# Performance work log

Hardware: AMD Instinct MI355X
Metric: run time of the kernel (lower is better)

## Reference

```python
import jax, jax.numpy as jnp
import numpy as np

BOUND = 1.0
MIN_NEAR = 0.05
NUM_STEPS = 64
UP_STEPS = 64
DENSITY_SCALE = 1.0
N_RAYS = 16384
HIDDEN = 64


def setup_inputs() -> dict:
    key = jax.random.key(0)
    ks = jax.random.split(key, 8)
    # cameras hover near z=2 looking roughly toward -z so rays hit the [-1,1]^3 AABB
    rays_o = jax.random.normal(ks[0], (N_RAYS, 3), jnp.float32) * 0.1 + jnp.array([0.0, 0.0, 2.0])
    rays_d = jax.random.normal(ks[1], (N_RAYS, 3), jnp.float32) * 0.2 + jnp.array([0.0, 0.0, -1.0])
    rays_d = rays_d / jnp.linalg.norm(rays_d, axis=-1, keepdims=True)
    W1 = jax.random.normal(ks[2], (3, HIDDEN), jnp.float32) / jnp.sqrt(3.0)
    b1 = jnp.zeros((HIDDEN,), jnp.float32)
    w_sigma = jax.random.normal(ks[3], (HIDDEN, 1), jnp.float32) / jnp.sqrt(float(HIDDEN))
    b_sigma = jnp.zeros((1,), jnp.float32)
    W_rgb = jax.random.normal(ks[4], (HIDDEN, 3), jnp.float32) / jnp.sqrt(float(HIDDEN))
    b_rgb = jnp.zeros((3,), jnp.float32)
    return {"rays_o": rays_o, "rays_d": rays_d, "W1": W1, "b1": b1,
            "w_sigma": w_sigma, "b_sigma": b_sigma, "W_rgb": W_rgb, "b_rgb": b_rgb}


def near_far_cube(rays_o, rays_d, bound, min_near):
    tmin = (-bound - rays_o) / (rays_d + 1e-15)
    tmax = (bound - rays_o) / (rays_d + 1e-15)
    near = jnp.max(jnp.minimum(tmin, tmax), axis=-1, keepdims=True)
    far = jnp.min(jnp.maximum(tmin, tmax), axis=-1, keepdims=True)
    miss = far < near
    near = jnp.where(miss, 1e9, near)
    far = jnp.where(miss, 1e9, far)
    near = jnp.maximum(near, min_near)
    return near, far


def sample_pdf(bins, weights, n_samples):
    # bins: [N, M+1], weights: [N, M]; deterministic (det=True) inverse-CDF sampling
    weights = weights + 1e-5
    pdf = weights / jnp.sum(weights, -1, keepdims=True)
    cdf = jnp.cumsum(pdf, -1)
    cdf = jnp.concatenate([jnp.zeros_like(cdf[..., :1]), cdf], -1)  # [N, M+1]
    u = jnp.linspace(0.5 / n_samples, 1.0 - 0.5 / n_samples, n_samples, dtype=cdf.dtype)
    u = jnp.broadcast_to(u, cdf.shape[:-1] + (n_samples,))
    inds = jax.vmap(lambda c, uu: jnp.searchsorted(c, uu, side='right'))(cdf, u)
    below = jnp.maximum(inds - 1, 0)
    above = jnp.minimum(inds, cdf.shape[-1] - 1)
    cdf_b = jnp.take_along_axis(cdf, below, -1)
    cdf_a = jnp.take_along_axis(cdf, above, -1)
    bins_b = jnp.take_along_axis(bins, below, -1)
    bins_a = jnp.take_along_axis(bins, above, -1)
    denom = cdf_a - cdf_b
    denom = jnp.where(denom < 1e-5, jnp.ones_like(denom), denom)
    t = (u - cdf_b) / denom
    return bins_b + t * (bins_a - bins_b)


def mlp(pts, W1, b1, w_sigma, b_sigma, W_rgb, b_rgb):
    h = jax.nn.relu(pts @ W1 + b1)                      # [N, T, HIDDEN]
    sigma = jax.nn.softplus(h @ w_sigma + b_sigma)[..., 0]  # [N, T]
    rgb = jax.nn.sigmoid(h @ W_rgb + b_rgb)             # [N, T, 3]
    return sigma, rgb


def alpha_composite_weights(z_vals, sigma, sample_dist):
    deltas = z_vals[..., 1:] - z_vals[..., :-1]
    deltas = jnp.concatenate([deltas, jnp.broadcast_to(sample_dist, deltas[..., :1].shape)], -1)
    alphas = 1.0 - jnp.exp(-deltas * DENSITY_SCALE * sigma)
    trans = jnp.cumprod(jnp.concatenate([jnp.ones_like(alphas[..., :1]), 1.0 - alphas + 1e-15], -1)[..., :-1], -1)
    return alphas * trans


def reference(rays_o, rays_d, W1, b1, w_sigma, b_sigma, W_rgb, b_rgb):
    rays_d = rays_d / jnp.linalg.norm(rays_d, axis=-1, keepdims=True)
    near, far = near_far_cube(rays_o, rays_d, BOUND, MIN_NEAR)  # [N,1]
    sample_dist = (far - near) / NUM_STEPS                      # [N,1]

    # coarse stratified (deterministic) samples
    z = jnp.linspace(0.0, 1.0, NUM_STEPS, dtype=rays_o.dtype)
    z_vals = near + (far - near) * z                            # [N,T]
    xyzs = rays_o[:, None, :] + rays_d[:, None, :] * z_vals[..., None]
    xyzs = jnp.clip(xyzs, -BOUND, BOUND)
    sigma, _ = mlp(xyzs, W1, b1, w_sigma, b_sigma, W_rgb, b_rgb)
    weights = alpha_composite_weights(z_vals, sigma, sample_dist)

    # inverse-CDF importance resampling (no-grad in original)
    z_mid = 0.5 * (z_vals[..., :-1] + z_vals[..., 1:])          # [N,T-1]
    new_z = sample_pdf(z_mid, weights[:, 1:-1], UP_STEPS)       # [N,UP]
    new_z = jax.lax.stop_gradient(new_z)

    z_all = jnp.sort(jnp.concatenate([z_vals, new_z], -1), -1)  # [N,T+UP]
    xyzs_all = rays_o[:, None, :] + rays_d[:, None, :] * z_all[..., None]
    xyzs_all = jnp.clip(xyzs_all, -BOUND, BOUND)
    sigma_all, rgb_all = mlp(xyzs_all, W1, b1, w_sigma, b_sigma, W_rgb, b_rgb)
    weights_all = alpha_composite_weights(z_all, sigma_all, sample_dist)

    weights_sum = jnp.sum(weights_all, -1)                      # [N]
    image = jnp.sum(weights_all[..., None] * rgb_all, axis=-2)  # [N,3]
    image = image + (1.0 - weights_sum)[..., None]              # white background
    return image
```

## Files before the change

kernel.cpp:

```cpp
#include <hip/hip_runtime.h>
#include <math.h>

#define WAVES_PER_BLOCK 4

typedef float v2f __attribute__((ext_vector_type(2)));
typedef float v4f __attribute__((ext_vector_type(4)));
typedef __fp16 fp16v2 __attribute__((ext_vector_type(2)));
typedef _Float16 half8 __attribute__((ext_vector_type(8)));

__device__ __forceinline__ v2f v2_fma(v2f a, v2f b, v2f c) {
    return __builtin_elementwise_fma(a, b, c);
}
__device__ __forceinline__ v2f v2_max0(v2f a) {
    return __builtin_elementwise_max(a, (v2f){0.0f, 0.0f});
}
__device__ __forceinline__ v2f v2_splat(float x) { return (v2f){x, x}; }

__device__ __forceinline__ float fast_rcp(float x) { return __builtin_amdgcn_rcpf(x); }

#define DPP_ROW_SHR(n)  (0x110 | (n))
#define DPP_WF_SL1      0x130
#define DPP_WF_SR1      0x138
#define DPP_ROW_BCAST15 0x142
#define DPP_ROW_BCAST31 0x143

template <int CTRL, int RM = 0xf, int BM = 0xf, bool BC = false>
__device__ __forceinline__ float fdpp(float old_, float src) {
    return __int_as_float(__builtin_amdgcn_update_dpp(
        __float_as_int(old_), __float_as_int(src), CTRL, RM, BM, BC));
}

__device__ __forceinline__ float lane63_bcast(float x) {
    return __int_as_float(__builtin_amdgcn_readlane(__float_as_int(x), 63));
}

__device__ __forceinline__ float scan_add_dpp(float x) {
    x += fdpp<DPP_ROW_SHR(1)>(0.0f, x);
    x += fdpp<DPP_ROW_SHR(2)>(0.0f, x);
    x += fdpp<DPP_ROW_SHR(4)>(0.0f, x);
    x += fdpp<DPP_ROW_SHR(8)>(0.0f, x);
    x += fdpp<DPP_ROW_BCAST15, 0xa>(0.0f, x);
    x += fdpp<DPP_ROW_BCAST31, 0xc>(0.0f, x);
    return x;
}
__device__ __forceinline__ float scan_mul_dpp(float x) {
    x *= fdpp<DPP_ROW_SHR(1)>(1.0f, x);
    x *= fdpp<DPP_ROW_SHR(2)>(1.0f, x);
    x *= fdpp<DPP_ROW_SHR(4)>(1.0f, x);
    x *= fdpp<DPP_ROW_SHR(8)>(1.0f, x);
    x *= fdpp<DPP_ROW_BCAST15, 0xa>(1.0f, x);
    x *= fdpp<DPP_ROW_BCAST31, 0xc>(1.0f, x);
    return x;
}
__device__ __forceinline__ float wave_sum_dpp(float x) {
    return lane63_bcast(scan_add_dpp(x));
}

__device__ __forceinline__ float softplus_f(float x) {
    return fmaxf(x, 0.0f) + __logf(1.0f + __expf(-fabsf(x)));
}
__device__ __forceinline__ float sigmoid_f(float x) {
    return fast_rcp(1.0f + __expf(-x));
}
__device__ __forceinline__ float clamp1(float x) {
    return fminf(fmaxf(x, -1.0f), 1.0f);
}

__device__ __forceinline__ int count_lt64(const float* a, float x) {
    int lo = 0, hi = 64;
    while (lo < hi) { int mid = (lo + hi) >> 1; if (a[mid] < x) lo = mid + 1; else hi = mid; }
    return lo;
}
__device__ __forceinline__ int count_le64(const float* a, float x) {
    int lo = 0, hi = 64;
    while (lo < hi) { int mid = (lo + hi) >> 1; if (a[mid] <= x) lo = mid + 1; else hi = mid; }
    return lo;
}

__device__ __forceinline__ half8 build_afrag(const v2f* cr, const v2f* mr, v2f zz, int q) {
    union { half8 h; fp16v2 p[4]; } af;
#pragma unroll
    for (int g4 = 0; g4 < 4; ++g4) {
        v2f hp = v2_max0(v2_fma(mr[q * 4 + g4], zz, cr[q * 4 + g4]));
        af.p[g4] = __builtin_amdgcn_cvt_pkrtz(hp.x, hp.y);
    }
    return af.h;
}

__global__ __launch_bounds__(WAVES_PER_BLOCK * 64, 4)
void nerf_render_kernel(const float* __restrict__ rays_o,
                        const float* __restrict__ rays_d,
                        const float* __restrict__ W1,
                        const float* __restrict__ b1,
                        const float* __restrict__ w_sigma,
                        const float* __restrict__ b_sigma,
                        const float* __restrict__ W_rgb,
                        const float* __restrict__ b_rgb,
                        float* __restrict__ out)
{
    const int tid  = threadIdx.x;
    const int lane = tid & 63;
    const int wv   = tid >> 6;
    const int ray  = blockIdx.x * WAVES_PER_BLOCK + wv;
    const int r15  = lane & 15;
    const int kgrp = lane >> 4;

    __shared__ float s_cm  [WAVES_PER_BLOCK][128];
    __shared__ float s_sig [WAVES_PER_BLOCK][64];
    __shared__ float s_zmid[WAVES_PER_BLOCK][64];
    __shared__ float s_cdf [WAVES_PER_BLOCK][64];
    __shared__ float s_zall[WAVES_PER_BLOCK][128];
    __shared__ float s_out [WAVES_PER_BLOCK][4 * 132];

    half8 bfrag[2];
#pragma unroll
    for (int q = 0; q < 2; ++q) {
#pragma unroll
        for (int j = 0; j < 8; ++j) {
            int k = q * 32 + kgrp * 8 + j;
            float wval = 0.0f;
            if (r15 == 0)      wval = w_sigma[k];
            else if (r15 < 4)  wval = W_rgb[3 * k + (r15 - 1)];
            bfrag[q][j] = (_Float16)wval;
        }
    }

    float ox = rays_o[ray * 3 + 0], oy = rays_o[ray * 3 + 1], oz = rays_o[ray * 3 + 2];
    float dx = rays_d[ray * 3 + 0], dy = rays_d[ray * 3 + 1], dz = rays_d[ray * 3 + 2];
    {
        float inv = __builtin_amdgcn_rsqf(dx * dx + dy * dy + dz * dz);
        dx *= inv; dy *= inv; dz *= inv;
    }

    float rx = fast_rcp(dx + 1e-15f);
    float ry = fast_rcp(dy + 1e-15f);
    float rz = fast_rcp(dz + 1e-15f);
    float t0x = (-1.0f - ox) * rx, t1x = (1.0f - ox) * rx;
    float t0y = (-1.0f - oy) * ry, t1y = (1.0f - oy) * ry;
    float t0z = (-1.0f - oz) * rz, t1z = (1.0f - oz) * rz;
    float nearv = fmaxf(fmaxf(fminf(t0x, t1x), fminf(t0y, t1y)), fminf(t0z, t1z));
    float farv  = fminf(fminf(fmaxf(t0x, t1x), fmaxf(t0y, t1y)), fmaxf(t0z, t1z));
    const bool miss = (farv < nearv);
    if (miss) { nearv = 1e9f; farv = 1e9f; }
    nearv = fmaxf(nearv, 0.05f);
    const float sample_dist = (farv - nearv) * (1.0f / 64.0f);

    const float bs0 = b_sigma[0];
    const float br0 = b_rgb[0], br1 = b_rgb[1], br2 = b_rgb[2];

    {
        float w1x = W1[lane], w1y = W1[64 + lane], w1z = W1[128 + lane];
        float eox = ox, eoy = oy, eoz = oz, msc = 1.0f;
        if (miss) {
            eox = clamp1(fmaf(dx, 1e9f, ox));
            eoy = clamp1(fmaf(dy, 1e9f, oy));
            eoz = clamp1(fmaf(dz, 1e9f, oz));
            msc = 0.0f;
        }
        float cj = fmaf(eox, w1x, fmaf(eoy, w1y, fmaf(eoz, w1z, b1[lane])));
        float mj = msc * fmaf(dx, w1x, fmaf(dy, w1y, dz * w1z));
        int g = (lane >> 1) * 4 + (lane & 1);
        s_cm[wv][g]     = cj;
        s_cm[wv][g + 2] = mj;
    }

    v2f cr[8], mr[8];
#pragma unroll
    for (int q = 0; q < 2; ++q) {
#pragma unroll
        for (int g4 = 0; g4 < 4; ++g4) {
            v4f g = *(const v4f*)&s_cm[wv][4 * (q * 16 + kgrp * 4 + g4)];
            cr[q * 4 + g4] = (v2f){g.x, g.y};
            mr[q * 4 + g4] = (v2f){g.z, g.w};
        }
    }

    const float biasv = (r15 == 0) ? bs0 : (r15 == 1) ? br0 : (r15 == 2) ? br1
                       : (r15 == 3) ? br2 : 0.0f;
    const v4f accInit = (v4f){biasv, biasv, biasv, biasv};

    const float stepz = (farv - nearv) * (1.0f / 63.0f);
#pragma unroll
    for (int mt = 0; mt < 4; ++mt) {
        float zs = fminf(fmaf(stepz, (float)(mt * 16 + r15), nearv), 6.0e4f);
        v2f zz = v2_splat(zs);
        v4f acc = accInit;
        acc = __builtin_amdgcn_mfma_f32_16x16x32_f16(build_afrag(cr, mr, zz, 0), bfrag[0], acc, 0, 0, 0);
        acc = __builtin_amdgcn_mfma_f32_16x16x32_f16(build_afrag(cr, mr, zz, 1), bfrag[1], acc, 0, 0, 0);
        if (r15 == 0) {
            *(v4f*)&s_sig[wv][mt * 16 + kgrp * 4] = acc;
        }
    }
    float sigma = softplus_f(s_sig[wv][lane]);

    float z = nearv + (farv - nearv) * ((float)lane * (1.0f / 63.0f));

    float z_next = fdpp<DPP_WF_SL1>(0.0f, z);
    float delta  = (lane < 63) ? (z_next - z) : sample_dist;
    float alpha  = 1.0f - __expf(-delta * sigma);
    float v      = 1.0f - alpha + 1e-15f;
    float incl   = scan_mul_dpp(v);
    float trans  = fdpp<DPP_WF_SR1>(1.0f, incl);
    float w = alpha * trans;

    float wgt = (lane >= 1 && lane <= 62) ? (w + 1e-5f) : 0.0f;
    float cumw = scan_add_dpp(wgt);
    float total = lane63_bcast(cumw);
    float cdf_incl = cumw * fast_rcp(total);

    float zmid = 0.5f * (z + z_next);
    s_zmid[wv][lane] = (lane < 63) ? zmid : 0.0f;
    s_cdf [wv][lane] = (lane < 63) ? cdf_incl : 2.0f;

    float u = 0.0078125f + (float)lane * 0.015625f;
    int ind = count_le64(s_cdf[wv], u);
    int below = ind - 1;
    int above = (ind < 62) ? ind : 62;
    float cb = s_cdf[wv][below], ca = s_cdf[wv][above];
    float bb = s_zmid[wv][below], ba = s_zmid[wv][above];
    float denom = ca - cb;
    if (denom < 1e-5f) denom = 1.0f;
    float t = (u - cb) * fast_rcp(denom);
    float nz = fmaf(t, ba - bb, bb);

    s_zmid[wv][lane] = z;
    s_cdf [wv][lane] = nz;
    int pa = lane + count_lt64(s_cdf [wv], z);
    int pb = lane + count_le64(s_zmid[wv], nz);
    s_zall[wv][pa] = z;
    s_zall[wv][pb] = nz;

    float za0 = s_zall[wv][2 * lane + 0];
    float za1 = s_zall[wv][2 * lane + 1];

#pragma unroll 2
    for (int mt = 0; mt < 8; ++mt) {
        const int Mbase = mt * 16;
        float zs = fminf(s_zall[wv][Mbase + r15], 6.0e4f);
        v2f zz = v2_splat(zs);
        v4f acc = accInit;
        acc = __builtin_amdgcn_mfma_f32_16x16x32_f16(build_afrag(cr, mr, zz, 0), bfrag[0], acc, 0, 0, 0);
        acc = __builtin_amdgcn_mfma_f32_16x16x32_f16(build_afrag(cr, mr, zz, 1), bfrag[1], acc, 0, 0, 0);
        if (r15 < 4) {
            *(v4f*)&s_out[wv][r15 * 132 + Mbase + kgrp * 4] = acc;
        }
    }

    v2f sgp = *(const v2f*)&s_out[wv][0 * 132 + 2 * lane];
    v2f rp  = *(const v2f*)&s_out[wv][1 * 132 + 2 * lane];
    v2f gp  = *(const v2f*)&s_out[wv][2 * 132 + 2 * lane];
    v2f bp  = *(const v2f*)&s_out[wv][3 * 132 + 2 * lane];

    float sg0 = softplus_f(sgp.x), sg1 = softplus_f(sgp.y);
    float r0 = sigmoid_f(rp.x),   r1 = sigmoid_f(rp.y);
    float g0 = sigmoid_f(gp.x),   g1 = sigmoid_f(gp.y);
    float bl0 = sigmoid_f(bp.x),  bl1 = sigmoid_f(bp.y);

    float zn0 = fdpp<DPP_WF_SL1>(0.0f, za0);
    float d0 = za1 - za0;
    float d1 = (lane < 63) ? (zn0 - za1) : sample_dist;
    float a0 = 1.0f - __expf(-d0 * sg0);
    float a1 = 1.0f - __expf(-d1 * sg1);
    float v0 = 1.0f - a0 + 1e-15f;
    float v1 = 1.0f - a1 + 1e-15f;
    float local = v0 * v1;
    float incl2 = scan_mul_dpp(local);
    float eprod = fdpp<DPP_WF_SR1>(1.0f, incl2);
    float w0 = a0 * eprod;
    float w1 = a1 * (eprod * v0);

    float wsum = wave_sum_dpp(w0 + w1);
    float rs   = wave_sum_dpp(fmaf(w0, r0,  w1 * r1));
    float gs   = wave_sum_dpp(fmaf(w0, g0,  w1 * g1));
    float bs   = wave_sum_dpp(fmaf(w0, bl0, w1 * bl1));

    if (lane == 0) {
        float bg = 1.0f - wsum;
        out[ray * 3 + 0] = rs + bg;
        out[ray * 3 + 1] = gs + bg;
        out[ray * 3 + 2] = bs + bg;
    }
}

extern "C" void kernel_launch(void* const* d_in, const int* in_sizes, int n_in,
                              void* d_out, int out_size, void* d_ws, size_t ws_size,
                              hipStream_t stream) {
    const float* rays_o  = (const float*)d_in[0];
    const float* rays_d  = (const float*)d_in[1];
    const float* W1      = (const float*)d_in[2];
    const float* b1      = (const float*)d_in[3];
    const float* w_sigma = (const float*)d_in[4];
    const float* b_sigma = (const float*)d_in[5];
    const float* W_rgb   = (const float*)d_in[6];
    const float* b_rgb   = (const float*)d_in[7];
    float* out = (float*)d_out;

    const int n_rays = in_sizes[0] / 3;
    dim3 grid((n_rays + WAVES_PER_BLOCK - 1) / WAVES_PER_BLOCK);
    dim3 block(WAVES_PER_BLOCK * 64);
    hipLaunchKernelGGL(nerf_render_kernel, grid, block, 0, stream,
                       rays_o, rays_d, W1, b1, w_sigma, b_sigma, W_rgb, b_rgb, out);
}
```

Baseline: 98.73 us.

## Replace LDS binary searches with DPP scatter-scan and bitonic merge in registers

The inverse-CDF search, which ran a per-lane binary search over shared memory, is replaced. Each CDF entry is turned into a bucket index for the uniform samples, the last lane per bucket is scattered, and a DPP max-scan then finds the 'below' index. The merge of coarse and fine z-values, which used two binary searches plus a shared-memory scatter, becomes a register bitonic merge over shuffles. The sorted values are fetched with __shfl during the MLP and compositing stages. This removes serialized LDS lookups and branches but adds many cross-lane shuffles, and the bucket-based search must match searchsorted exactly at tie boundaries.

```diff
diff --git a/kernel.cpp b/kernel.cpp
--- a/kernel.cpp
+++ b/kernel.cpp
@@ -28,6 +28,10 @@
 __device__ __forceinline__ float fdpp(float old_, float src) {
     return __int_as_float(__builtin_amdgcn_update_dpp(
         __float_as_int(old_), __float_as_int(src), CTRL, RM, BM, BC));
+}
+template <int CTRL, int RM = 0xf, int BM = 0xf, bool BC = false>
+__device__ __forceinline__ int idpp(int old_, int src) {
+    return __builtin_amdgcn_update_dpp(old_, src, CTRL, RM, BM, BC);
 }
 
 __device__ __forceinline__ float lane63_bcast(float x) {
@@ -55,6 +59,17 @@
 __device__ __forceinline__ float wave_sum_dpp(float x) {
     return lane63_bcast(scan_add_dpp(x));
 }
+__device__ __forceinline__ int imax2(int a, int b) { return a > b ? a : b; }
+__device__ __forceinline__ int imax_scan_dpp(int x) {
+    const int NEG = (int)0x80000000;
+    x = imax2(x, idpp<DPP_ROW_SHR(1)>(NEG, x));
+    x = imax2(x, idpp<DPP_ROW_SHR(2)>(NEG, x));
+    x = imax2(x, idpp<DPP_ROW_SHR(4)>(NEG, x));
+    x = imax2(x, idpp<DPP_ROW_SHR(8)>(NEG, x));
+    x = imax2(x, idpp<DPP_ROW_BCAST15, 0xa>(NEG, x));
+    x = imax2(x, idpp<DPP_ROW_BCAST31, 0xc>(NEG, x));
+    return x;
+}
 
 __device__ __forceinline__ float softplus_f(float x) {
     return fmaxf(x, 0.0f) + __logf(1.0f + __expf(-fabsf(x)));
@@ -66,15 +81,14 @@
     return fminf(fmaxf(x, -1.0f), 1.0f);
 }
 
-__device__ __forceinline__ int count_lt64(const float* a, float x) {
-    int lo = 0, hi = 64;
-    while (lo < hi) { int mid = (lo + hi) >> 1; if (a[mid] < x) lo = mid + 1; else hi = mid; }
-    return lo;
-}
-__device__ __forceinline__ int count_le64(const float* a, float x) {
-    int lo = 0, hi = 64;
-    while (lo < hi) { int mid = (lo + hi) >> 1; if (a[mid] <= x) lo = mid + 1; else hi = mid; }
-    return lo;
+__device__ __forceinline__ void bstage(float& a, float& b, int d, int lane) {
+    float av = __shfl_xor(a, d, 64);
+    float bv = __shfl_xor(b, d, 64);
+    bool up = (lane & d) != 0;
+    float alo = fminf(a, av), ahi = fmaxf(a, av);
+    float blo = fminf(b, bv), bhi = fmaxf(b, bv);
+    a = up ? ahi : alo;
+    b = up ? bhi : blo;
 }
 
 __device__ __forceinline__ half8 build_afrag(const v2f* cr, const v2f* mr, v2f zz, int q) {
@@ -105,12 +119,10 @@
     const int r15  = lane & 15;
     const int kgrp = lane >> 4;
 
-    __shared__ float s_cm  [WAVES_PER_BLOCK][128];
-    __shared__ float s_sig [WAVES_PER_BLOCK][64];
-    __shared__ float s_zmid[WAVES_PER_BLOCK][64];
-    __shared__ float s_cdf [WAVES_PER_BLOCK][64];
-    __shared__ float s_zall[WAVES_PER_BLOCK][128];
-    __shared__ float s_out [WAVES_PER_BLOCK][4 * 132];
+    __shared__ float s_cm [WAVES_PER_BLOCK][128];
+    __shared__ int   s_scr[WAVES_PER_BLOCK][64];
+    __shared__ float s_sig[WAVES_PER_BLOCK][64];
+    __shared__ float s_out[WAVES_PER_BLOCK][4 * 132];
 
     half8 bfrag[2];
 #pragma unroll
@@ -208,35 +220,47 @@
     float total = lane63_bcast(cumw);
     float cdf_incl = cumw * fast_rcp(total);
 
-    float zmid = 0.5f * (z + z_next);
-    s_zmid[wv][lane] = (lane < 63) ? zmid : 0.0f;
-    s_cdf [wv][lane] = (lane < 63) ? cdf_incl : 2.0f;
-
-    float u = 0.0078125f + (float)lane * 0.015625f;
-    int ind = count_le64(s_cdf[wv], u);
-    int below = ind - 1;
-    int above = (ind < 62) ? ind : 62;
-    float cb = s_cdf[wv][below], ca = s_cdf[wv][above];
-    float bb = s_zmid[wv][below], ba = s_zmid[wv][above];
+    float cdfv  = (lane < 63) ? cdf_incl : 2.0f;
+    float zmidv = (lane < 63) ? (0.5f * (z + z_next)) : 0.0f;
+
+    int s = (int)ceilf(fmaf(64.0f, cdfv, -0.5f));
+    s = s < 0 ? 0 : (s > 64 ? 64 : s);
+    int snext = idpp<DPP_WF_SL1>(65, s);
+    bool glast = (snext > s) && (s < 64);
+
+    s_scr[wv][lane] = -1;
+    if (glast) s_scr[wv][s] = lane;
+    int below = imax_scan_dpp(s_scr[wv][lane]);
+    int above = below + 1; if (above > 62) above = 62;
+
+    float cb = __shfl(cdfv,  below, 64);
+    float ca = __shfl(cdfv,  above, 64);
+    float bb = __shfl(zmidv, below, 64);
+    float ba = __shfl(zmidv, above, 64);
     float denom = ca - cb;
     if (denom < 1e-5f) denom = 1.0f;
-    float t = (u - cb) * fast_rcp(denom);
+    float t = (__shfl(cdfv, 0, 64) * 0.0f + (0.0078125f + (float)lane * 0.015625f) - cb) * fast_rcp(denom);
     float nz = fmaf(t, ba - bb, bb);
 
-    s_zmid[wv][lane] = z;
-    s_cdf [wv][lane] = nz;
-    int pa = lane + count_lt64(s_cdf [wv], z);
-    int pb = lane + count_le64(s_zmid[wv], nz);
-    s_zall[wv][pa] = z;
-    s_zall[wv][pb] = nz;
-
-    float za0 = s_zall[wv][2 * lane + 0];
-    float za1 = s_zall[wv][2 * lane + 1];
+    float r0v = z;
+    float r1v = __shfl(nz, 63 - lane, 64);
+    {
+        float lo = fminf(r0v, r1v), hi = fmaxf(r0v, r1v);
+        r0v = lo; r1v = hi;
+    }
+    bstage(r0v, r1v, 32, lane);
+    bstage(r0v, r1v, 16, lane);
+    bstage(r0v, r1v,  8, lane);
+    bstage(r0v, r1v,  4, lane);
+    bstage(r0v, r1v,  2, lane);
+    bstage(r0v, r1v,  1, lane);
 
 #pragma unroll 2
     for (int mt = 0; mt < 8; ++mt) {
         const int Mbase = mt * 16;
-        float zs = fminf(s_zall[wv][Mbase + r15], 6.0e4f);
+        float zraw = (mt < 4) ? __shfl(r0v, Mbase + r15, 64)
+                              : __shfl(r1v, (Mbase - 64) + r15, 64);
+        float zs = fminf(zraw, 6.0e4f);
         v2f zz = v2_splat(zs);
         v4f acc = accInit;
         acc = __builtin_amdgcn_mfma_f32_16x16x32_f16(build_afrag(cr, mr, zz, 0), bfrag[0], acc, 0, 0, 0);
@@ -246,33 +270,39 @@
         }
     }
 
+    int i0 = 2 * lane, i1 = 2 * lane + 1;
+    float a0r = __shfl(r0v, i0 & 63, 64), a0s = __shfl(r1v, i0 & 63, 64);
+    float a1r = __shfl(r0v, i1 & 63, 64), a1s = __shfl(r1v, i1 & 63, 64);
+    float za0 = (i0 < 64) ? a0r : a0s;
+    float za1 = (i1 < 64) ? a1r : a1s;
+
     v2f sgp = *(const v2f*)&s_out[wv][0 * 132 + 2 * lane];
     v2f rp  = *(const v2f*)&s_out[wv][1 * 132 + 2 * lane];
     v2f gp  = *(const v2f*)&s_out[wv][2 * 132 + 2 * lane];
     v2f bp  = *(const v2f*)&s_out[wv][3 * 132 + 2 * lane];
 
     float sg0 = softplus_f(sgp.x), sg1 = softplus_f(sgp.y);
-    float r0 = sigmoid_f(rp.x),   r1 = sigmoid_f(rp.y);
-    float g0 = sigmoid_f(gp.x),   g1 = sigmoid_f(gp.y);
-    float bl0 = sigmoid_f(bp.x),  bl1 = sigmoid_f(bp.y);
+    float r0c = sigmoid_f(rp.x),   r1c = sigmoid_f(rp.y);
+    float g0c = sigmoid_f(gp.x),   g1c = sigmoid_f(gp.y);
+    float b0c = sigmoid_f(bp.x),   b1c = sigmoid_f(bp.y);
 
     float zn0 = fdpp<DPP_WF_SL1>(0.0f, za0);
     float d0 = za1 - za0;
     float d1 = (lane < 63) ? (zn0 - za1) : sample_dist;
-    float a0 = 1.0f - __expf(-d0 * sg0);
-    float a1 = 1.0f - __expf(-d1 * sg1);
-    float v0 = 1.0f - a0 + 1e-15f;
-    float v1 = 1.0f - a1 + 1e-15f;
+    float aa0 = 1.0f - __expf(-d0 * sg0);
+    float aa1 = 1.0f - __expf(-d1 * sg1);
+    float v0 = 1.0f - aa0 + 1e-15f;
+    float v1 = 1.0f - aa1 + 1e-15f;
     float local = v0 * v1;
     float incl2 = scan_mul_dpp(local);
     float eprod = fdpp<DPP_WF_SR1>(1.0f, incl2);
-    float w0 = a0 * eprod;
-    float w1 = a1 * (eprod * v0);
+    float w0 = aa0 * eprod;
+    float w1 = aa1 * (eprod * v0);
 
     float wsum = wave_sum_dpp(w0 + w1);
-    float rs   = wave_sum_dpp(fmaf(w0, r0,  w1 * r1));
-    float gs   = wave_sum_dpp(fmaf(w0, g0,  w1 * g1));
-    float bs   = wave_sum_dpp(fmaf(w0, bl0, w1 * bl1));
+    float rs   = wave_sum_dpp(fmaf(w0, r0c, w1 * r1c));
+    float gs   = wave_sum_dpp(fmaf(w0, g0c, w1 * g1c));
+    float bs   = wave_sum_dpp(fmaf(w0, b0c, w1 * b1c));
 
     if (lane == 0) {
         float bg = 1.0f - wsum;
```

Result: no change. 98.01 us (-0.7%).
